# Kernel tuning notes

Measured on AMD Instinct MI355X. Metric: run time of the kernel, lower is better.

The kernel has to match this reference:

```python
import jax, jax.numpy as jnp
import numpy as np

ALPHA = 0.2  # LeakyReLU negative slope (init arg `alpha`)
N, F_IN, F_OUT = 8192, 512, 256


def setup_inputs() -> dict:
    key = jax.random.key(0)
    k1, k2, k3, k4 = jax.random.split(key, 4)
    x = jax.random.normal(k1, (N, F_IN), dtype=jnp.float32)
    adj = jax.random.randint(k2, (N, N), 0, 2, dtype=jnp.int32)
    W = jax.random.normal(k3, (F_IN, F_OUT), dtype=jnp.float32) * (1.0 / np.sqrt(F_IN))
    a = jax.random.normal(k4, (2 * F_OUT, 1), dtype=jnp.float32) * (1.0 / np.sqrt(F_IN))
    return {"x": x, "adj": adj, "W": W, "a": a}


def reference(x, adj, W, a):
    h = x @ W  # [N, F_OUT]
    f_out = W.shape[1]
    # e[i,j] = LeakyReLU(a1 . h_i + a2 . h_j); computed without the O(N^2*2F) concat
    f1 = h @ a[:f_out, 0]   # [N]
    f2 = h @ a[f_out:, 0]   # [N]
    s = f1[:, None] + f2[None, :]  # [N, N]
    e = jnp.where(s >= 0, s, ALPHA * s)
    # Faithful to the source bug: -9e15 * zeros_like == zeros, so masked entries are 0.0
    att = jnp.where(adj > 0, e, jnp.zeros((), dtype=e.dtype))
    att = jax.nn.softmax(att, axis=1)
    # dropout is identity in eval mode
    h_prime = att @ h  # [N, F_OUT]
    return jax.nn.elu(h_prime)  # concat=True branch
```

## Files before the change

### kernel.cpp

```cpp
#include <hip/hip_runtime.h>
#include <stdint.h>

#define NN 8192
#define FIN 512
#define FOUT 256
#define ALPHA 0.2f
#define KSPLIT 8

typedef float f32x4 __attribute__((ext_vector_type(4)));
typedef short s16x8 __attribute__((ext_vector_type(8)));

__device__ __forceinline__ uint16_t f2bf(float f) {
  union { float f; uint32_t u; } v; v.f = f;
  uint32_t u = v.u + 0x7fffu + ((v.u >> 16) & 1u);
  return (uint16_t)(u >> 16);
}

__global__ __launch_bounds__(256) void k_wa_prep(const float* __restrict__ W,
                                                 const float* __restrict__ a,
                                                 uint16_t* __restrict__ wt,
                                                 float* __restrict__ wa1, float* __restrict__ wa2) {
  int bx = blockIdx.x;
  int tid = threadIdx.x;
  if (bx < 128) {
    int idx = bx * 256 + tid;
    int f  = idx >> 7;
    int k4 = (idx & 127) * 4;
    ushort4 o;
    o.x = f2bf(W[(size_t)(k4 + 0) * FOUT + f]);
    o.y = f2bf(W[(size_t)(k4 + 1) * FOUT + f]);
    o.z = f2bf(W[(size_t)(k4 + 2) * FOUT + f]);
    o.w = f2bf(W[(size_t)(k4 + 3) * FOUT + f]);
    *(ushort4*)(wt + (size_t)f * FIN + k4) = o;
  } else {
    __shared__ float a1[256], a2[256];
    a1[tid] = a[tid];
    a2[tid] = a[tid + 256];
    __syncthreads();
    int m = (bx - 128) * 256 + tid;
    const float* wrow = W + (size_t)m * FOUT;
    float s1 = 0.f, s2 = 0.f;
    for (int k = 0; k < FOUT; k += 4) {
      f32x4 v = *(const f32x4*)(wrow + k);
#pragma unroll
      for (int i = 0; i < 4; i++) {
        s1 += v[i] * a1[k + i];
        s2 += v[i] * a2[k + i];
      }
    }
    wa1[m] = s1; wa2[m] = s2;
  }
}

__global__ __launch_bounds__(256) void k_f1f2(const float* __restrict__ x,
                                              const float* __restrict__ wa1,
                                              const float* __restrict__ wa2,
                                              float* __restrict__ f1, float* __restrict__ f2,
                                              uint16_t* __restrict__ xb,
                                              float* __restrict__ l_arr) {
  __shared__ float s1[512], s2[512];
  int tid = threadIdx.x;
  if (tid < 4) l_arr[blockIdx.x * 4 + tid] = 0.f;
  s1[tid] = wa1[tid]; s1[tid + 256] = wa1[tid + 256];
  s2[tid] = wa2[tid]; s2[tid + 256] = wa2[tid + 256];
  __syncthreads();
  int w = tid >> 6, l = tid & 63;
  int row = blockIdx.x * 4 + w;
  const float* xr = x + (size_t)row * FIN + l * 8;
  f32x4 v0 = *(const f32x4*)xr;
  f32x4 v1 = *(const f32x4*)(xr + 4);
  uint4 pk;
  pk.x = (uint32_t)f2bf(v0[0]) | ((uint32_t)f2bf(v0[1]) << 16);
  pk.y = (uint32_t)f2bf(v0[2]) | ((uint32_t)f2bf(v0[3]) << 16);
  pk.z = (uint32_t)f2bf(v1[0]) | ((uint32_t)f2bf(v1[1]) << 16);
  pk.w = (uint32_t)f2bf(v1[2]) | ((uint32_t)f2bf(v1[3]) << 16);
  *(uint4*)(xb + (size_t)row * FIN + l * 8) = pk;
  int kb = l * 8;
  float d1 = 0.f, d2 = 0.f;
#pragma unroll
  for (int i = 0; i < 4; i++) {
    d1 += v0[i] * s1[kb + i] + v1[i] * s1[kb + 4 + i];
    d2 += v0[i] * s2[kb + i] + v1[i] * s2[kb + 4 + i];
  }
#pragma unroll
  for (int off = 32; off; off >>= 1) {
    d1 += __shfl_down(d1, off);
    d2 += __shfl_down(d2, off);
  }
  if (l == 0) { f1[row] = d1; f2[row] = d2; }
}

__global__ __launch_bounds__(256, 2) void k_gemm_ht(const uint16_t* __restrict__ xb,
                                                    const uint16_t* __restrict__ wt,
                                                    uint16_t* __restrict__ ht) {
  __shared__ uint16_t Xs[64][40];
  __shared__ uint16_t Ws[64][40];
  __shared__ uint16_t T[64][72];
  int i0 = blockIdx.x * 64;
  int f0 = blockIdx.y * 64;
  int tid = threadIdx.x;
  int w = tid >> 6, l = tid & 63;
  int q = l >> 4, r16 = l & 15;
  f32x4 acc[4];
#pragma unroll
  for (int b = 0; b < 4; b++) acc[b] = (f32x4)0.f;

  int srow = tid >> 2, sch = tid & 3;
  for (int k0 = 0; k0 < FIN; k0 += 32) {
    uint4 xv = *(const uint4*)(xb + (size_t)(i0 + srow) * FIN + k0 + sch * 8);
    uint4 wv = *(const uint4*)(wt + (size_t)(f0 + srow) * FIN + k0 + sch * 8);
    *(uint4*)(&Xs[srow][sch * 8]) = xv;
    *(uint4*)(&Ws[srow][sch * 8]) = wv;
    __syncthreads();
    s16x8 A = *(const s16x8*)(&Xs[w * 16 + r16][q * 8]);
    s16x8 B[4];
#pragma unroll
    for (int b = 0; b < 4; b++) B[b] = *(const s16x8*)(&Ws[b * 16 + r16][q * 8]);
#pragma unroll
    for (int b = 0; b < 4; b++)
      acc[b] = __builtin_amdgcn_mfma_f32_16x16x32_bf16(A, B[b], acc[b], 0, 0, 0);
    __syncthreads();
  }
#pragma unroll
  for (int b = 0; b < 4; b++)
#pragma unroll
    for (int reg = 0; reg < 4; reg++)
      T[w * 16 + q * 4 + reg][b * 16 + r16] = f2bf(acc[b][reg]);
  __syncthreads();
#pragma unroll
  for (int p = 0; p < 2; p++) {
    int idx = tid + p * 256;
    int fr = idx >> 3, ic8 = idx & 7;
    s16x8 v;
#pragma unroll
    for (int j = 0; j < 8; j++) v[j] = (short)T[ic8 * 8 + j][fr];
    *(s16x8*)(ht + (size_t)(f0 + fr) * NN + i0 + ic8 * 8) = v;
  }
}

__global__ __launch_bounds__(256, 2) void k_att(const int* __restrict__ adj,
                                                const uint16_t* __restrict__ ht,
                                                const float* __restrict__ f1,
                                                const float* __restrict__ f2,
                                                float* __restrict__ l_arr,
                                                float* __restrict__ part) {
  __shared__ uint16_t Ps[64][72];
  __shared__ uint16_t Hs[256][72];
  int i0 = blockIdx.x * 64;
  int jbase = blockIdx.y * (NN / KSPLIT);
  int tid = threadIdx.x;
  int w = tid >> 6, l = tid & 63;
  int q = l >> 4, r16 = l & 15;
  int prow = tid >> 2, pch = tid & 3;
  int srow = tid >> 3, sch = tid & 7;
  float f1i = f1[i0 + prow];
  float lsum = 0.f;
  f32x4 acc[4][4];
#pragma unroll
  for (int a = 0; a < 4; a++)
#pragma unroll
    for (int b = 0; b < 4; b++) acc[a][b] = (f32x4)0.f;

  for (int s = 0; s < NN / KSPLIT; s += 64) {
    int j0 = jbase + s;
    uint4 hv[8];
#pragma unroll
    for (int p = 0; p < 8; p++)
      hv[p] = *(const uint4*)(ht + (size_t)(p * 32 + srow) * NN + j0 + sch * 8);
    const int* ap = adj + (size_t)(i0 + prow) * NN + j0 + pch * 16;
    int4 A0 = *(const int4*)ap;
    int4 A1 = *(const int4*)(ap + 4);
    int4 A2 = *(const int4*)(ap + 8);
    int4 A3 = *(const int4*)(ap + 12);
    f32x4 F0 = *(const f32x4*)(f2 + j0 + pch * 16);
    f32x4 F1 = *(const f32x4*)(f2 + j0 + pch * 16 + 4);
    f32x4 F2 = *(const f32x4*)(f2 + j0 + pch * 16 + 8);
    f32x4 F3 = *(const f32x4*)(f2 + j0 + pch * 16 + 12);
    s16x8 pv0, pv1;
#define PCOMP(dst, Ac, Fc, kk) { float s_ = f1i + (Fc); float e_ = s_ > 0.f ? s_ : ALPHA * s_; \
                                 float p_ = ((Ac) != 0) ? __expf(e_) : 1.0f; lsum += p_; \
                                 dst[kk] = (short)f2bf(p_); }
    PCOMP(pv0, A0.x, F0[0], 0); PCOMP(pv0, A0.y, F0[1], 1);
    PCOMP(pv0, A0.z, F0[2], 2); PCOMP(pv0, A0.w, F0[3], 3);
    PCOMP(pv0, A1.x, F1[0], 4); PCOMP(pv0, A1.y, F1[1], 5);
    PCOMP(pv0, A1.z, F1[2], 6); PCOMP(pv0, A1.w, F1[3], 7);
    PCOMP(pv1, A2.x, F2[0], 0); PCOMP(pv1, A2.y, F2[1], 1);
    PCOMP(pv1, A2.z, F2[2], 2); PCOMP(pv1, A2.w, F2[3], 3);
    PCOMP(pv1, A3.x, F3[0], 4); PCOMP(pv1, A3.y, F3[1], 5);
    PCOMP(pv1, A3.z, F3[2], 6); PCOMP(pv1, A3.w, F3[3], 7);
#undef PCOMP
    *(s16x8*)(&Ps[prow][pch * 16]) = pv0;
    *(s16x8*)(&Ps[prow][pch * 16 + 8]) = pv1;
#pragma unroll
    for (int p = 0; p < 8; p++)
      *(uint4*)(&Hs[p * 32 + srow][sch * 8]) = hv[p];
    __syncthreads();
#pragma unroll
    for (int c = 0; c < 2; c++) {
      s16x8 Af[4], Bf[4];
#pragma unroll
      for (int a = 0; a < 4; a++) Af[a] = *(const s16x8*)(&Ps[a * 16 + r16][c * 32 + q * 8]);
#pragma unroll
      for (int b = 0; b < 4; b++) Bf[b] = *(const s16x8*)(&Hs[w * 64 + b * 16 + r16][c * 32 + q * 8]);
#pragma unroll
      for (int a = 0; a < 4; a++)
#pragma unroll
        for (int b = 0; b < 4; b++)
          acc[a][b] = __builtin_amdgcn_mfma_f32_16x16x32_bf16(Af[a], Bf[b], acc[a][b], 0, 0, 0);
    }
    __syncthreads();
  }

  lsum += __shfl_down(lsum, 2);
  lsum += __shfl_down(lsum, 1);
  if (pch == 0) atomicAdd(&l_arr[i0 + prow], lsum);

  float* pb = part + (size_t)blockIdx.y * ((size_t)NN * FOUT);
#pragma unroll
  for (int a = 0; a < 4; a++)
#pragma unroll
    for (int b = 0; b < 4; b++)
#pragma unroll
      for (int reg = 0; reg < 4; reg++) {
        int row = i0 + a * 16 + q * 4 + reg;
        int col = w * 64 + b * 16 + r16;
        pb[(size_t)row * FOUT + col] = acc[a][b][reg];
      }
}

__global__ __launch_bounds__(256) void k_combine(const float* __restrict__ part,
                                                 const float* __restrict__ l_arr,
                                                 float* __restrict__ out) {
  int idx = (blockIdx.x * 256 + threadIdx.x) * 4;
  float r = 1.0f / l_arr[idx >> 8];
  f32x4 sum = (f32x4)0.f;
#pragma unroll
  for (int p = 0; p < KSPLIT; p++)
    sum += *(const f32x4*)(part + (size_t)p * (NN * FOUT) + idx);
  f32x4 o;
#pragma unroll
  for (int i = 0; i < 4; i++) {
    float v = sum[i] * r;
    o[i] = v > 0.f ? v : (__expf(v) - 1.f);
  }
  *(f32x4*)(out + idx) = o;
}

extern "C" void kernel_launch(void* const* d_in, const int* in_sizes, int n_in,
                              void* d_out, int out_size, void* d_ws, size_t ws_size,
                              hipStream_t stream) {
  const float* x   = (const float*)d_in[0];
  const int*   adj = (const int*)d_in[1];
  const float* W   = (const float*)d_in[2];
  const float* a   = (const float*)d_in[3];
  float* out = (float*)d_out;

  char* ws = (char*)d_ws;
  float*    wa1   = (float*)ws;
  float*    wa2   = wa1 + 512;
  float*    f1    = wa2 + 512;
  float*    f2    = f1 + NN;
  float*    l_arr = f2 + NN;
  uint16_t* wt    = (uint16_t*)(l_arr + NN);
  uint16_t* xb    = wt + (size_t)FOUT * FIN;
  uint16_t* ht    = xb + (size_t)NN * FIN;
  float*    part  = (float*)(ht + (size_t)NN * FOUT);

  k_wa_prep<<<130, 256, 0, stream>>>(W, a, wt, wa1, wa2);
  k_f1f2<<<NN / 4, 256, 0, stream>>>(x, wa1, wa2, f1, f2, xb, l_arr);
  k_gemm_ht<<<dim3(NN / 64, FOUT / 64), 256, 0, stream>>>(xb, wt, ht);
  k_att<<<dim3(NN / 64, KSPLIT), 256, 0, stream>>>(adj, ht, f1, f2, l_arr, part);
  k_combine<<<NN * FOUT / 1024, 256, 0, stream>>>(part, l_arr, out);
}
```

Measured before the change: 464.0 us.

## Halve attention K-split, deepen gemm K-tile, use nontemporal combine loads

Measured after the change: 437.1 us. 1.06x faster.

```diff
diff --git a/kernel.cpp b/kernel.cpp
--- a/kernel.cpp
+++ b/kernel.cpp
@@ -5,7 +5,7 @@
 #define FIN 512
 #define FOUT 256
 #define ALPHA 0.2f
-#define KSPLIT 8
+#define KSPLIT 4
 
 typedef float f32x4 __attribute__((ext_vector_type(4)));
 typedef short s16x8 __attribute__((ext_vector_type(8)));
@@ -93,8 +93,8 @@
 __global__ __launch_bounds__(256, 2) void k_gemm_ht(const uint16_t* __restrict__ xb,
                                                     const uint16_t* __restrict__ wt,
                                                     uint16_t* __restrict__ ht) {
-  __shared__ uint16_t Xs[64][40];
-  __shared__ uint16_t Ws[64][40];
+  __shared__ uint16_t Xs[64][72];
+  __shared__ uint16_t Ws[64][72];
   __shared__ uint16_t T[64][72];
   int i0 = blockIdx.x * 64;
   int f0 = blockIdx.y * 64;
@@ -106,19 +106,28 @@
   for (int b = 0; b < 4; b++) acc[b] = (f32x4)0.f;
 
   int srow = tid >> 2, sch = tid & 3;
-  for (int k0 = 0; k0 < FIN; k0 += 32) {
-    uint4 xv = *(const uint4*)(xb + (size_t)(i0 + srow) * FIN + k0 + sch * 8);
-    uint4 wv = *(const uint4*)(wt + (size_t)(f0 + srow) * FIN + k0 + sch * 8);
-    *(uint4*)(&Xs[srow][sch * 8]) = xv;
-    *(uint4*)(&Ws[srow][sch * 8]) = wv;
-    __syncthreads();
-    s16x8 A = *(const s16x8*)(&Xs[w * 16 + r16][q * 8]);
-    s16x8 B[4];
-#pragma unroll
-    for (int b = 0; b < 4; b++) B[b] = *(const s16x8*)(&Ws[b * 16 + r16][q * 8]);
-#pragma unroll
-    for (int b = 0; b < 4; b++)
-      acc[b] = __builtin_amdgcn_mfma_f32_16x16x32_bf16(A, B[b], acc[b], 0, 0, 0);
+  for (int k0 = 0; k0 < FIN; k0 += 64) {
+    const uint16_t* xp = xb + (size_t)(i0 + srow) * FIN + k0;
+    const uint16_t* wp = wt + (size_t)(f0 + srow) * FIN + k0;
+    uint4 xv0 = *(const uint4*)(xp + sch * 8);
+    uint4 xv1 = *(const uint4*)(xp + 32 + sch * 8);
+    uint4 wv0 = *(const uint4*)(wp + sch * 8);
+    uint4 wv1 = *(const uint4*)(wp + 32 + sch * 8);
+    *(uint4*)(&Xs[srow][sch * 8]) = xv0;
+    *(uint4*)(&Xs[srow][32 + sch * 8]) = xv1;
+    *(uint4*)(&Ws[srow][sch * 8]) = wv0;
+    *(uint4*)(&Ws[srow][32 + sch * 8]) = wv1;
+    __syncthreads();
+#pragma unroll
+    for (int c = 0; c < 2; c++) {
+      s16x8 A = *(const s16x8*)(&Xs[w * 16 + r16][c * 32 + q * 8]);
+      s16x8 B[4];
+#pragma unroll
+      for (int b = 0; b < 4; b++) B[b] = *(const s16x8*)(&Ws[b * 16 + r16][c * 32 + q * 8]);
+#pragma unroll
+      for (int b = 0; b < 4; b++)
+        acc[b] = __builtin_amdgcn_mfma_f32_16x16x32_bf16(A, B[b], acc[b], 0, 0, 0);
+    }
     __syncthreads();
   }
 #pragma unroll
@@ -233,17 +242,17 @@
                                                  float* __restrict__ out) {
   int idx = (blockIdx.x * 256 + threadIdx.x) * 4;
   float r = 1.0f / l_arr[idx >> 8];
-  f32x4 sum = (f32x4)0.f;
-#pragma unroll
-  for (int p = 0; p < KSPLIT; p++)
-    sum += *(const f32x4*)(part + (size_t)p * (NN * FOUT) + idx);
+  f32x4 v0 = __builtin_nontemporal_load((const f32x4*)(part + 0 * (size_t)(NN * FOUT) + idx));
+  f32x4 v1 = __builtin_nontemporal_load((const f32x4*)(part + 1 * (size_t)(NN * FOUT) + idx));
+  f32x4 v2 = __builtin_nontemporal_load((const f32x4*)(part + 2 * (size_t)(NN * FOUT) + idx));
+  f32x4 v3 = __builtin_nontemporal_load((const f32x4*)(part + 3 * (size_t)(NN * FOUT) + idx));
   f32x4 o;
 #pragma unroll
   for (int i = 0; i < 4; i++) {
-    float v = sum[i] * r;
+    float v = (v0[i] + v1[i] + v2[i] + v3[i]) * r;
     o[i] = v > 0.f ? v : (__expf(v) - 1.f);
   }
-  *(f32x4*)(out + idx) = o;
+  __builtin_nontemporal_store(o, (f32x4*)(out + idx));
 }
 
 extern "C" void kernel_launch(void* const* d_in, const int* in_sizes, int n_in,
```
